# Performance work log

Measured on AMD Instinct MI355X. Metric: run time of the kernel, lower is better.

The kernel has to match this reference:

```python
import jax, jax.numpy as jnp
import numpy as np

B, N, F = 64, 128, 4
H = 100


def setup_inputs() -> dict:
    key = jax.random.key(0)
    ks = jax.random.split(key, 8)
    x = jax.random.normal(ks[0], (B, N, F), dtype=jnp.float32)
    in_hitnr = jax.random.randint(ks[1], (B, N), 0, N, dtype=jnp.int32)
    W1 = jax.random.normal(ks[2], (2 * F, H), dtype=jnp.float32) * (1.0 / np.sqrt(2 * F))
    b1 = jax.random.normal(ks[3], (H,), dtype=jnp.float32) * 0.01
    W2 = jax.random.normal(ks[4], (H, H), dtype=jnp.float32) * (1.0 / np.sqrt(H))
    b2 = jax.random.normal(ks[5], (H,), dtype=jnp.float32) * 0.01
    W3 = jax.random.normal(ks[6], (H, 1), dtype=jnp.float32) * (1.0 / np.sqrt(H))
    b3 = jax.random.normal(ks[7], (1,), dtype=jnp.float32) * 0.01
    return {"x": x, "in_hitnr": in_hitnr, "W1": W1, "b1": b1,
            "W2": W2, "b2": b2, "W3": W3, "b3": b3}


def reference(x, in_hitnr, W1, b1, W2, b2, W3, b3):
    n = x.shape[1]
    # itertools.combinations(range(n), 2) == lexicographic upper-triangle order
    i1, i2 = jnp.triu_indices(n, k=1)  # each [num_pairs]
    # pairwise gather + concat: [B, P, 2F]
    pairs = jnp.concatenate([x[:, i1], x[:, i2]], axis=-1)
    h = pairs @ W1 + b1                 # [B, P, 100]
    h = h @ W2 + b2                     # [B, P, 100]
    h = jax.nn.relu(h)                  # ReLU applied AFTER second linear (as in source)
    out = h @ W3 + b3                   # [B, P, 1]
    out = jax.nn.sigmoid(out)
    return jnp.squeeze(out, axis=-1)    # [B, P]
```

## Files before the change

kernel.cpp:

```cpp
#include <hip/hip_runtime.h>
#include <math.h>


namespace {
constexpr int B_    = 64;
constexpr int N_    = 128;
constexpr int H_    = 100;
constexpr int TILE  = 32;
constexpr int NT    = N_ / TILE;
constexpr int NTP   = NT * (NT + 1) / 2;
constexpr int PAIRS = N_ * (N_ - 1) / 2;
constexpr int FROW  = 12;
constexpr int FW3   = H_ * FROW;
constexpr int FB3   = FW3 + H_;
constexpr int FTOT  = 1304;
}

__device__ __align__(16) float g_fold2[FTOT];

__global__ __launch_bounds__(128)
void fold_weights(const float* __restrict__ W1, const float* __restrict__ b1,
                  const float* __restrict__ W2, const float* __restrict__ b2,
                  const float* __restrict__ W3, const float* __restrict__ b3)
{
    const int idx = blockIdx.x * 128 + threadIdx.x;
    if (idx < 800) {
        const int k = idx / H_;
        const int h = idx - k * H_;
        const float* w1r = W1 + k * H_;
        float s = 0.f;
        #pragma unroll 5
        for (int j = 0; j < H_; ++j) s = fmaf(w1r[j], W2[j * H_ + h], s);
        g_fold2[h * FROW + k] = s;
    } else if (idx < 900) {
        const int h = idx - 800;
        float s = b2[h];
        #pragma unroll 5
        for (int j = 0; j < H_; ++j) s = fmaf(b1[j], W2[j * H_ + h], s);
        g_fold2[h * FROW + 8] = s;
    } else if (idx < 1000) {
        g_fold2[FW3 + (idx - 900)] = W3[idx - 900];
    } else if (idx == 1000) {
        g_fold2[FB3] = b3[0];
    }
}

__global__ __launch_bounds__(256)
void pairnet(const float* __restrict__ x, float* __restrict__ out)
{
    __shared__ __align__(16) float fold_s[FTOT];
    __shared__ __align__(16) float U_s[50 * TILE * 2];
    __shared__ __align__(16) float V_s[50 * TILE * 2];

    const int t   = threadIdx.x;
    const int blk = blockIdx.x;
    const int b   = blk / NTP;
    int rem = blk - b * NTP;
    int ti = 0;
    while (rem >= NT - ti) { rem -= NT - ti; ++ti; }
    const int tj = ti + rem;
    const int i0 = ti * TILE, j0 = tj * TILE;

    {
        const float4* gf4 = (const float4*)g_fold2;
        float4* fs4 = (float4*)fold_s;
        fs4[t & 255] = gf4[t & 255];
        if (t < FTOT / 4 - 256) fs4[256 + t] = gf4[256 + t];
    }
    const int r = t & 31;
    const float4 xi = ((const float4*)x)[b * N_ + i0 + r];
    const float4 xj = ((const float4*)x)[b * N_ + j0 + r];
    __syncthreads();

    for (int k = 0; k < 7; ++k) {
        const int idx = t + k * 256;
        if (idx < 1600) {
            const int h2 = idx >> 5;
            const float* row0 = &fold_s[(2 * h2) * FROW];
            const float* row1 = &fold_s[(2 * h2 + 1) * FROW];
            const float4 a0 = *(const float4*)(row0);
            const float4 b0 = *(const float4*)(row0 + 4);
            const float4 a1 = *(const float4*)(row1);
            const float4 b1v = *(const float4*)(row1 + 4);
            float2 u, v;
            u.x = row0[8] + xi.x*a0.x + xi.y*a0.y + xi.z*a0.z + xi.w*a0.w;
            u.y = row1[8] + xi.x*a1.x + xi.y*a1.y + xi.z*a1.z + xi.w*a1.w;
            v.x =           xj.x*b0.x + xj.y*b0.y + xj.z*b0.z + xj.w*b0.w;
            v.y =           xj.x*b1v.x + xj.y*b1v.y + xj.z*b1v.z + xj.w*b1v.w;
            *(float2*)&U_s[h2 * 64 + r * 2] = u;
            *(float2*)&V_s[h2 * 64 + r * 2] = v;
        }
    }
    __syncthreads();

    const int iq = t >> 4;
    const int jq = t & 15;
    const int ia = 2 * iq, ja = 2 * jq;
    float a00 = 0.f, a01 = 0.f, a10 = 0.f, a11 = 0.f;
    #pragma unroll 2
    for (int h2 = 0; h2 < 50; ++h2) {
        const float2 w = *(const float2*)&fold_s[FW3 + 2 * h2];
        const float4 u = *(const float4*)&U_s[h2 * 64 + ia * 2];
        const float4 v = *(const float4*)&V_s[h2 * 64 + ja * 2];
        a00 = fmaf(w.x, fmaxf(u.x + v.x, 0.f), fmaf(w.y, fmaxf(u.y + v.y, 0.f), a00));
        a01 = fmaf(w.x, fmaxf(u.x + v.z, 0.f), fmaf(w.y, fmaxf(u.y + v.w, 0.f), a01));
        a10 = fmaf(w.x, fmaxf(u.z + v.x, 0.f), fmaf(w.y, fmaxf(u.w + v.y, 0.f), a10));
        a11 = fmaf(w.x, fmaxf(u.z + v.z, 0.f), fmaf(w.y, fmaxf(u.w + v.w, 0.f), a11));
    }

    const float b3v = fold_s[FB3];
    float* outb = out + b * PAIRS;
    const float accs[2][2] = {{a00, a01}, {a10, a11}};
    #pragma unroll
    for (int da = 0; da < 2; ++da) {
        #pragma unroll
        for (int dc = 0; dc < 2; ++dc) {
            const int gi = i0 + ia + da;
            const int gj = j0 + ja + dc;
            if (gi < gj) {
                const int p = (gi * (2 * N_ - gi - 1)) / 2 + (gj - gi - 1);
                outb[p] = 1.f / (1.f + __expf(-(accs[da][dc] + b3v)));
            }
        }
    }
}

extern "C" void kernel_launch(void* const* d_in, const int* in_sizes, int n_in,
                              void* d_out, int out_size, void* d_ws, size_t ws_size,
                              hipStream_t stream) {
    const float* x  = (const float*)d_in[0];
    const float* W1 = (const float*)d_in[2];
    const float* b1 = (const float*)d_in[3];
    const float* W2 = (const float*)d_in[4];
    const float* b2 = (const float*)d_in[5];
    const float* W3 = (const float*)d_in[6];
    const float* b3 = (const float*)d_in[7];
    float* out = (float*)d_out;

    fold_weights<<<dim3(8),        dim3(128), 0, stream>>>(W1, b1, W2, b2, W3, b3);
    pairnet     <<<dim3(B_ * NTP), dim3(256), 0, stream>>>(x, out);
}
```

Measured before the change: 85.62 us.

## Fuse weight folding into pair kernel, recomputing folded weights per block

Removes the separate fold_weights launch. Each block now loads W2 and W1 into shared memory and computes the folded W1·W2 and bias terms itself before building U/V. This saves one kernel launch and the global round-trip, at the cost of redundant 40KB loads and about 90K FMAs per block across 640 blocks, plus more shared memory (about 50KB), which may reduce occupancy.

```diff
diff --git a/kernel.cpp b/kernel.cpp
--- a/kernel.cpp
+++ b/kernel.cpp
@@ -14,43 +14,22 @@
 constexpr int FW3   = H_ * FROW;
 constexpr int FB3   = FW3 + H_;
 constexpr int FTOT  = 1304;
-}
-
-__device__ __align__(16) float g_fold2[FTOT];
-
-__global__ __launch_bounds__(128)
-void fold_weights(const float* __restrict__ W1, const float* __restrict__ b1,
-                  const float* __restrict__ W2, const float* __restrict__ b2,
-                  const float* __restrict__ W3, const float* __restrict__ b3)
-{
-    const int idx = blockIdx.x * 128 + threadIdx.x;
-    if (idx < 800) {
-        const int k = idx / H_;
-        const int h = idx - k * H_;
-        const float* w1r = W1 + k * H_;
-        float s = 0.f;
-        #pragma unroll 5
-        for (int j = 0; j < H_; ++j) s = fmaf(w1r[j], W2[j * H_ + h], s);
-        g_fold2[h * FROW + k] = s;
-    } else if (idx < 900) {
-        const int h = idx - 800;
-        float s = b2[h];
-        #pragma unroll 5
-        for (int j = 0; j < H_; ++j) s = fmaf(b1[j], W2[j * H_ + h], s);
-        g_fold2[h * FROW + 8] = s;
-    } else if (idx < 1000) {
-        g_fold2[FW3 + (idx - 900)] = W3[idx - 900];
-    } else if (idx == 1000) {
-        g_fold2[FB3] = b3[0];
-    }
+constexpr int SCR   = 11200;
 }
 
 __global__ __launch_bounds__(256)
-void pairnet(const float* __restrict__ x, float* __restrict__ out)
+void pairnet_one(const float* __restrict__ x,
+                 const float* __restrict__ W1, const float* __restrict__ b1,
+                 const float* __restrict__ W2, const float* __restrict__ b2,
+                 const float* __restrict__ W3, const float* __restrict__ b3,
+                 float* __restrict__ out)
 {
     __shared__ __align__(16) float fold_s[FTOT];
-    __shared__ __align__(16) float U_s[50 * TILE * 2];
-    __shared__ __align__(16) float V_s[50 * TILE * 2];
+    __shared__ __align__(16) float scratch[SCR];
+    float* const W2s = scratch;
+    float* const W1T = scratch + 10000;
+    float* const U_s = scratch;
+    float* const V_s = scratch + 3200;
 
     const int t   = threadIdx.x;
     const int blk = blockIdx.x;
@@ -61,31 +40,64 @@
     const int tj = ti + rem;
     const int i0 = ti * TILE, j0 = tj * TILE;
 
-    {
-        const float4* gf4 = (const float4*)g_fold2;
-        float4* fs4 = (float4*)fold_s;
-        fs4[t & 255] = gf4[t & 255];
-        if (t < FTOT / 4 - 256) fs4[256 + t] = gf4[256 + t];
-    }
     const int r = t & 31;
     const float4 xi = ((const float4*)x)[b * N_ + i0 + r];
     const float4 xj = ((const float4*)x)[b * N_ + j0 + r];
+
+    {
+        const float4* W2g = (const float4*)W2;
+        float4* W2s4 = (float4*)W2s;
+        #pragma unroll
+        for (int k = 0; k < 10; ++k) {
+            const int idx = t + k * 256;
+            if (idx < 2500) W2s4[idx] = W2g[idx];
+        }
+        for (int idx = t; idx < 800; idx += 256) {
+            const int k = idx / 100, j = idx - k * 100;
+            W1T[j * FROW + k] = W1[idx];
+        }
+        if (t < 100) W1T[t * FROW + 8] = b1[t];
+        if (t < 100) fold_s[FW3 + t] = W3[t];
+        if (t == 0)  fold_s[FB3] = b3[0];
+    }
     __syncthreads();
 
+    if (t < 200) {
+        const int half = t / 100;
+        const int h    = t - half * 100;
+        float a0 = 0.f, a1 = 0.f, a2 = 0.f, a3 = 0.f;
+        float ac = (half == 0) ? b2[h] : 0.f;
+        #pragma unroll 4
+        for (int j = 0; j < H_; ++j) {
+            const float  w2 = W2s[j * H_ + h];
+            const float4 w1 = *(const float4*)&W1T[j * FROW + 4 * half];
+            a0 = fmaf(w2, w1.x, a0);
+            a1 = fmaf(w2, w1.y, a1);
+            a2 = fmaf(w2, w1.z, a2);
+            a3 = fmaf(w2, w1.w, a3);
+            if (half == 0) ac = fmaf(w2, W1T[j * FROW + 8], ac);
+        }
+        float* row = &fold_s[h * FROW + 4 * half];
+        row[0] = a0; row[1] = a1; row[2] = a2; row[3] = a3;
+        if (half == 0) fold_s[h * FROW + 8] = ac;
+    }
+    __syncthreads();
+
+    #pragma unroll
     for (int k = 0; k < 7; ++k) {
         const int idx = t + k * 256;
         if (idx < 1600) {
             const int h2 = idx >> 5;
             const float* row0 = &fold_s[(2 * h2) * FROW];
             const float* row1 = &fold_s[(2 * h2 + 1) * FROW];
-            const float4 a0 = *(const float4*)(row0);
-            const float4 b0 = *(const float4*)(row0 + 4);
-            const float4 a1 = *(const float4*)(row1);
+            const float4 a0  = *(const float4*)(row0);
+            const float4 b0  = *(const float4*)(row0 + 4);
+            const float4 a1  = *(const float4*)(row1);
             const float4 b1v = *(const float4*)(row1 + 4);
             float2 u, v;
-            u.x = row0[8] + xi.x*a0.x + xi.y*a0.y + xi.z*a0.z + xi.w*a0.w;
-            u.y = row1[8] + xi.x*a1.x + xi.y*a1.y + xi.z*a1.z + xi.w*a1.w;
-            v.x =           xj.x*b0.x + xj.y*b0.y + xj.z*b0.z + xj.w*b0.w;
+            u.x = row0[8] + xi.x*a0.x  + xi.y*a0.y  + xi.z*a0.z  + xi.w*a0.w;
+            u.y = row1[8] + xi.x*a1.x  + xi.y*a1.y  + xi.z*a1.z  + xi.w*a1.w;
+            v.x =           xj.x*b0.x  + xj.y*b0.y  + xj.z*b0.z  + xj.w*b0.w;
             v.y =           xj.x*b1v.x + xj.y*b1v.y + xj.z*b1v.z + xj.w*b1v.w;
             *(float2*)&U_s[h2 * 64 + r * 2] = u;
             *(float2*)&V_s[h2 * 64 + r * 2] = v;
@@ -137,6 +149,6 @@
     const float* b3 = (const float*)d_in[7];
     float* out = (float*)d_out;
 
-    fold_weights<<<dim3(8),        dim3(128), 0, stream>>>(W1, b1, W2, b2, W3, b3);
-    pairnet     <<<dim3(B_ * NTP), dim3(256), 0, stream>>>(x, out);
+    pairnet_one<<<dim3(B_ * NTP), dim3(256), 0, stream>>>(
+        x, W1, b1, W2, b2, W3, b3, out);
 }
```

Result: no change. 85.12 us (-0.6%).
